# Kernel optimization log

Measured on AMD Instinct MI355X. Metric: run time of the kernel, lower is better.

## Reference

```python
import jax, jax.numpy as jnp
import numpy as np

D_MODEL = 1024
N_HEADS = 16
HEAD_DIM = D_MODEL // N_HEADS
ROPE_BASE = 10000.0
NEG_INF = -1.0e9


def rotate_half(x):
    # interleaved pairs: (-x2_i, x1_i) re-flattened to last dim
    x1 = x[..., ::2]
    x2 = x[..., 1::2]
    return jnp.stack((-x2, x1), axis=-1).reshape(x.shape)


def rope_sin_cos(seq_len, head_dim, dtype):
    inv_freq = 1.0 / (ROPE_BASE ** (jnp.arange(0, head_dim, 2, dtype=jnp.float32) / head_dim))
    t = jnp.arange(seq_len, dtype=jnp.float32)
    freqs = jnp.einsum('i,j->ij', t, inv_freq)          # [T, hd/2]
    emb = jnp.concatenate((freqs, freqs), axis=-1)       # [T, hd]
    return jnp.sin(emb).astype(dtype), jnp.cos(emb).astype(dtype)


def apply_rope(x, sin, cos):
    # x: [B, H, T, hd]; sin/cos: [T, hd]
    return x * cos[None, None] + rotate_half(x) * sin[None, None]


def setup_inputs() -> dict:
    key = jax.random.key(0)
    ks = jax.random.split(key, 9)
    B, T, D = 2, 2048, D_MODEL
    q = jax.random.normal(ks[0], (B, T, D), dtype=jnp.float32)
    k = jax.random.normal(ks[1], (B, T, D), dtype=jnp.float32)
    v = jax.random.normal(ks[2], (B, T, D), dtype=jnp.float32)
    # causal additive mask, broadcastable over [B, H, Tq, Tk]
    causal = jnp.triu(jnp.full((T, T), NEG_INF, dtype=jnp.float32), k=1)
    attn_mask = causal[None, None]
    key_padding_mask = jax.random.uniform(ks[3], (B, T)) < 0.05
    scale = 1.0 / np.sqrt(D)
    Wq = jax.random.normal(ks[4], (D, D), dtype=jnp.float32) * scale
    Wk = jax.random.normal(ks[5], (D, D), dtype=jnp.float32) * scale
    Wv = jax.random.normal(ks[6], (D, D), dtype=jnp.float32) * scale
    Wo = jax.random.normal(ks[7], (D, D), dtype=jnp.float32) * scale
    return {"q": q, "k": k, "v": v, "attn_mask": attn_mask,
            "key_padding_mask": key_padding_mask,
            "Wq": Wq, "Wk": Wk, "Wv": Wv, "Wo": Wo}


def reference(q, k, v, attn_mask, key_padding_mask, Wq, Wk, Wv, Wo):
    B, Tq, _ = q.shape
    Tk = k.shape[1]
    H, hd = N_HEADS, HEAD_DIM
    # projections (nn.Linear: x @ W.T), split heads -> [B, H, T, hd]
    qh = (q @ Wq.T).reshape(B, Tq, H, hd).transpose(0, 2, 1, 3)
    kh = (k @ Wk.T).reshape(B, Tk, H, hd).transpose(0, 2, 1, 3)
    vh = (v @ Wv.T).reshape(B, Tk, H, hd).transpose(0, 2, 1, 3)
    sin_q, cos_q = rope_sin_cos(Tq, hd, q.dtype)
    sin_k, cos_k = rope_sin_cos(Tk, hd, k.dtype)
    qh = apply_rope(qh, sin_q, cos_q)
    kh = apply_rope(kh, sin_k, cos_k)
    scores = jnp.einsum('bhqd,bhkd->bhqk', qh, kh) / np.sqrt(hd)
    scores = scores + attn_mask
    scores = jnp.where(key_padding_mask[:, None, None, :], NEG_INF, scores)
    attn = jax.nn.softmax(scores, axis=-1)
    out = jnp.einsum('bhqk,bhkd->bhqd', attn, vh)
    out = out.transpose(0, 2, 1, 3).reshape(B, Tq, H * hd)
    return out @ Wo.T
```

## Files before the change

kernel.cpp:

```cpp
#include <hip/hip_runtime.h>
#include <stdint.h>

typedef __bf16 bf16x8 __attribute__((ext_vector_type(8)));
typedef float f32x4 __attribute__((ext_vector_type(4)));
typedef float f32x16 __attribute__((ext_vector_type(16)));

#define NEG_BIG2 (-1.442695040e9f)
#define SC_LOG2  (0.180336880f)

__device__ __forceinline__ unsigned short f2b(float f) {
  union { float f; unsigned int u; } c; c.f = f;
  unsigned int u = c.u;
  u += 0x7FFFu + ((u >> 16) & 1u);
  return (unsigned short)(u >> 16);
}
__device__ __forceinline__ float b2f(unsigned short h) {
  union { unsigned int u; float f; } c; c.u = ((unsigned int)h) << 16;
  return c.f;
}
__device__ __forceinline__ unsigned int pk2(float a, float b) {
  __bf16 x = (__bf16)a, y = (__bf16)b;
  unsigned short xu, yu;
  __builtin_memcpy(&xu, &x, 2);
  __builtin_memcpy(&yu, &y, 2);
  return (unsigned)xu | ((unsigned)yu << 16);
}
__device__ __forceinline__ float ex2(float x) {
  float r; asm("v_exp_f32 %0, %1" : "=v"(r) : "v"(x)); return r;
}

typedef const __attribute__((address_space(1))) unsigned int ga_u32;
typedef __attribute__((address_space(3))) unsigned int ls_u32;
__device__ __forceinline__ void gld16(const void* g, void* l) {
  __builtin_amdgcn_global_load_lds((ga_u32*)g, (ls_u32*)l, 16, 0, 0);
}

__device__ __forceinline__ void swap_pair(unsigned a, unsigned b, int hi,
                                          unsigned& lo_out, unsigned& hi_out) {
#if __has_builtin(__builtin_amdgcn_permlane32_swap)
  auto r = __builtin_amdgcn_permlane32_swap(a, b, false, false);
  lo_out = r[0]; hi_out = r[1];
#else
  unsigned pa = __shfl_xor(a, 32), pb = __shfl_xor(b, 32);
  lo_out = hi ? pb : a;
  hi_out = hi ? b : pa;
#endif
}

__device__ __constant__ unsigned char job_tab[24] = {
  7, 47, 63, 46, 62, 6, 45, 61, 44, 60, 5, 43,
  59, 42, 58, 4, 41, 57, 40, 56, 3, 2, 1, 0};

__global__ void rope_table_k(float* __restrict__ sin_t, float* __restrict__ cos_t) {
  int i = blockIdx.x * blockDim.x + threadIdx.x;
  int t = i >> 6, d = i & 63, f = d & 31;
  double inv = exp(-((double)(2 * f) / 64.0) * log(10000.0));
  double ang = (double)t * inv;
  sin_t[i] = (float)sin(ang);
  cos_t[i] = (float)cos(ang);
}

__global__ void detect_mask_k(const unsigned int* __restrict__ kpm, int* __restrict__ flag) {
  unsigned int v = 0;
  for (int i = threadIdx.x; i < 1024; i += 256) v |= kpm[i];
  if (v & ~1u) atomicOr(flag, 1);
}

__global__ void mask_pack_k(const void* __restrict__ kpm, const int* __restrict__ mflag,
                            unsigned long long* __restrict__ pmask) {
  const int w = threadIdx.x >> 6, lane = threadIdx.x & 63;
  const int bytes = *mflag;
  for (int i = w; i < 64; i += 4) {
    int b = i >> 5, kb = i & 31;
    int idx = b * 2048 + kb * 64 + lane;
    int pad = bytes ? (int)((const unsigned char*)kpm)[idx] : ((const int*)kpm)[idx];
    unsigned long long pm = __ballot(pad != 0);
    if (lane == 0) pmask[i] = pm;
  }
}

__global__ void convw_k(const float* __restrict__ Wq, const float* __restrict__ Wk,
                        const float* __restrict__ Wv, const float* __restrict__ Wo,
                        unsigned short* __restrict__ Wb) {
  size_t g = (size_t)blockIdx.x * 256 + threadIdx.x;
  size_t i8 = g * 8;
  int t = (int)(i8 >> 20);
  const float* src = (t == 0 ? Wq : t == 1 ? Wk : t == 2 ? Wv : Wo) + (i8 & 1048575);
  float4 a = *(const float4*)src, c = *(const float4*)(src + 4);
  uint4 o = { pk2(a.x, a.y), pk2(a.z, a.w), pk2(c.x, c.y), pk2(c.z, c.w) };
  *(uint4*)&Wb[i8] = o;
}

__global__ void conv_in_k(const float* __restrict__ q, const float* __restrict__ k,
                          const float* __restrict__ v, unsigned short* __restrict__ qb,
                          unsigned short* __restrict__ kb, unsigned short* __restrict__ vb) {
  size_t g = (size_t)blockIdx.x * 256 + threadIdx.x;
  size_t i8 = g * 8;
  int t = (int)(i8 >> 22);
  size_t off = i8 & 4194303;
  const float* src = (t == 0 ? q : t == 1 ? k : v) + off;
  unsigned short* dst = (t == 0 ? qb : t == 1 ? kb : vb) + off;
  float4 a = *(const float4*)src, c = *(const float4*)(src + 4);
  uint4 o = { pk2(a.x, a.y), pk2(a.z, a.w), pk2(c.x, c.y), pk2(c.z, c.w) };
  *(uint4*)dst = o;
}

template<bool ABF>
__global__ __launch_bounds__(256) void qkv_k(const void* __restrict__ A0,
                                             const void* __restrict__ A1,
                                             const void* __restrict__ A2,
                                             const unsigned short* __restrict__ Wb,
                                             unsigned short* __restrict__ qh,
                                             unsigned short* __restrict__ kh,
                                             unsigned short* __restrict__ vt) {
  const int z = blockIdx.z;
  const void* Ap = (z == 0) ? A0 : (z == 1) ? A1 : A2;
  const unsigned short* Wp = Wb + (size_t)z * 1048576;
  unsigned short* outp = (z == 0) ? qh : (z == 1) ? kh : vt;

  __shared__ unsigned short As[128 * 32];
  __shared__ unsigned short Bs[128 * 32];
  const int M0 = blockIdx.x * 128, N0 = blockIdx.y * 128;
  const int tid = threadIdx.x, lane = tid & 63, w = tid >> 6;
  const int wr = w >> 1, wc = w & 1;
  const int lrow = lane & 15, lgrp = lane >> 4;

  const f32x4 Z4 = {0.f, 0.f, 0.f, 0.f};
  f32x4 acc[4][4];
#pragma unroll
  for (int i = 0; i < 4; ++i)
#pragma unroll
    for (int j = 0; j < 4; ++j) acc[i][j] = Z4;

  for (int kt = 0; kt < 1024; kt += 32) {
    __syncthreads();
    if (ABF) {
      const unsigned short* Ab = (const unsigned short*)Ap;
#pragma unroll
      for (int i = 0; i < 2; ++i) {
        const unsigned short* gA = Ab +
            (size_t)(M0 + i * 64 + w * 16 + (lane >> 2)) * 1024 + kt + (lane & 3) * 8;
        gld16(gA, &As[i * 2048 + w * 512]);
      }
    } else {
      const int row = tid >> 1, half = tid & 1;
      const float* ap = (const float*)Ap + (size_t)(M0 + row) * 1024 + kt + half * 16;
      float4 f0 = *(const float4*)ap, f1 = *(const float4*)(ap + 4);
      float4 f2 = *(const float4*)(ap + 8), f3 = *(const float4*)(ap + 12);
      uint4 u0 = { pk2(f0.x, f0.y), pk2(f0.z, f0.w), pk2(f1.x, f1.y), pk2(f1.z, f1.w) };
      uint4 u1 = { pk2(f2.x, f2.y), pk2(f2.z, f2.w), pk2(f3.x, f3.y), pk2(f3.z, f3.w) };
      *(uint4*)&As[row * 32 + half * 16] = u0;
      *(uint4*)&As[row * 32 + half * 16 + 8] = u1;
    }
#pragma unroll
    for (int i = 0; i < 2; ++i) {
      const unsigned short* gB = Wp +
          (size_t)(N0 + i * 64 + w * 16 + (lane >> 2)) * 1024 + kt + (lane & 3) * 8;
      gld16(gB, &Bs[i * 2048 + w * 512]);
    }
    __syncthreads();
    bf16x8 af[4], bfv[4];
#pragma unroll
    for (int m = 0; m < 4; ++m)
      af[m] = *(const bf16x8*)&As[(wr * 64 + m * 16 + lrow) * 32 + lgrp * 8];
#pragma unroll
    for (int n = 0; n < 4; ++n)
      bfv[n] = *(const bf16x8*)&Bs[(wc * 64 + n * 16 + lrow) * 32 + lgrp * 8];
    __builtin_amdgcn_s_setprio(1);
#pragma unroll
    for (int m = 0; m < 4; ++m)
#pragma unroll
      for (int n = 0; n < 4; ++n)
        acc[m][n] = __builtin_amdgcn_mfma_f32_16x16x32_bf16(af[m], bfv[n], acc[m][n], 0, 0, 0);
    __builtin_amdgcn_s_setprio(0);
  }

#pragma unroll
  for (int mi = 0; mi < 4; ++mi)
#pragma unroll
    for (int ni = 0; ni < 4; ++ni) {
      const int m = M0 + wr * 64 + mi * 16 + lgrp * 4;
      const int n = N0 + wc * 64 + ni * 16 + lrow;
      const int b = m >> 11, t = m & 2047;
      if (z < 2) {
        unsigned short* o = outp +
            ((size_t)(b * 16 + (n >> 6)) * 2048 + t) * 64 + (n & 63);
#pragma unroll
        for (int r = 0; r < 4; ++r) o[(size_t)r * 64] = f2b(acc[mi][ni][r]);
      } else {
        unsigned short* o = outp +
            ((size_t)(b * 16 + (n >> 6)) * 64 + (n & 63)) * 2048 + t;
        *(ushort4*)o = make_ushort4(f2b(acc[mi][ni][0]), f2b(acc[mi][ni][1]),
                                    f2b(acc[mi][ni][2]), f2b(acc[mi][ni][3]));
      }
    }
}

__global__ __launch_bounds__(256) void gemm_o_k(const unsigned short* __restrict__ Ab,
                                                const unsigned short* __restrict__ Wp,
                                                float* __restrict__ outp) {
  __shared__ unsigned short As[64 * 32];
  __shared__ unsigned short Bs[128 * 32];
  const int M0 = blockIdx.x * 64, N0 = blockIdx.y * 128;
  const int tid = threadIdx.x, lane = tid & 63, w = tid >> 6;
  const int wr = w >> 1, wc = w & 1;
  const int lrow = lane & 15, lgrp = lane >> 4;

  const f32x4 Z4 = {0.f, 0.f, 0.f, 0.f};
  f32x4 acc[2][4];
#pragma unroll
  for (int i = 0; i < 2; ++i)
#pragma unroll
    for (int j = 0; j < 4; ++j) acc[i][j] = Z4;

  for (int kt = 0; kt < 1024; kt += 32) {
    __syncthreads();
    {
      const unsigned short* gA = Ab +
          (size_t)(M0 + w * 16 + (lane >> 2)) * 1024 + kt + (lane & 3) * 8;
      gld16(gA, &As[w * 512]);
    }
#pragma unroll
    for (int i = 0; i < 2; ++i) {
      const unsigned short* gB = Wp +
          (size_t)(N0 + i * 64 + w * 16 + (lane >> 2)) * 1024 + kt + (lane & 3) * 8;
      gld16(gB, &Bs[i * 2048 + w * 512]);
    }
    __syncthreads();
    bf16x8 af[2], bfv[4];
#pragma unroll
    for (int m = 0; m < 2; ++m)
      af[m] = *(const bf16x8*)&As[(wr * 32 + m * 16 + lrow) * 32 + lgrp * 8];
#pragma unroll
    for (int n = 0; n < 4; ++n)
      bfv[n] = *(const bf16x8*)&Bs[(wc * 64 + n * 16 + lrow) * 32 + lgrp * 8];
    __builtin_amdgcn_s_setprio(1);
#pragma unroll
    for (int m = 0; m < 2; ++m)
#pragma unroll
      for (int n = 0; n < 4; ++n)
        acc[m][n] = __builtin_amdgcn_mfma_f32_16x16x32_bf16(af[m], bfv[n], acc[m][n], 0, 0, 0);
    __builtin_amdgcn_s_setprio(0);
  }

#pragma unroll
  for (int mi = 0; mi < 2; ++mi)
#pragma unroll
    for (int ni = 0; ni < 4; ++ni) {
      const int m = M0 + wr * 32 + mi * 16 + lgrp * 4;
      const int n = N0 + wc * 64 + ni * 16 + lrow;
      float* o = outp + (size_t)m * 1024 + n;
#pragma unroll
      for (int r = 0; r < 4; ++r) o[(size_t)r * 1024] = acc[mi][ni][r];
    }
}

__global__ void rope_apply_k(unsigned short* __restrict__ qh, unsigned short* __restrict__ kh,
                             const float* __restrict__ sin_t, const float* __restrict__ cos_t) {
  const size_t per = (size_t)2 * 16 * 2048 * 16;
  size_t gid = (size_t)blockIdx.x * blockDim.x + threadIdx.x;
  if (gid >= 2 * per) return;
  const bool is_q = gid < per;
  unsigned short* base = is_q ? qh : kh;
  const float sc = is_q ? SC_LOG2 : 1.0f;
  size_t g = is_q ? gid : gid - per;
  const int t = (int)((g >> 4) & 2047);
  const int d0 = ((int)g & 15) * 4;
  ushort4 x = ((ushort4*)base)[g];
  const float4 s4 = *(const float4*)&sin_t[t * 64 + d0];
  const float4 c4 = *(const float4*)&cos_t[t * 64 + d0];
  float x0 = b2f(x.x), x1 = b2f(x.y), x2 = b2f(x.z), x3 = b2f(x.w);
  ushort4 o;
  o.x = f2b((x0 * c4.x - x1 * s4.x) * sc);
  o.y = f2b((x1 * c4.y + x0 * s4.y) * sc);
  o.z = f2b((x2 * c4.z - x3 * s4.z) * sc);
  o.w = f2b((x3 * c4.w + x2 * s4.w) * sc);
  ((ushort4*)base)[g] = o;
}

__global__ __launch_bounds__(256, 2) void attn_k(
    const unsigned short* __restrict__ qh, const unsigned short* __restrict__ kh,
    const unsigned short* __restrict__ vt, const unsigned long long* __restrict__ pmask,
    unsigned short* __restrict__ ao, float* __restrict__ Op, float* __restrict__ Ml,
    const int mode) {
  const int bid = blockIdx.x;
  int bh, tile, half = 0, split = 0;
  if (mode) {
    const unsigned char j = job_tab[bid >> 5];
    bh = bid & 31;
    tile = j & 15; half = (j >> 4) & 1; split = j >> 5;
  } else {
    const int x = bid & 7, g = bid >> 3;
    bh = x * 4 + (g & 3);
    tile = 15 - (g >> 2);
  }
  const int b = bh >> 4, h = bh & 15;
  const int tid = threadIdx.x, lane = tid & 63, w = tid >> 6;
  const int ln31 = lane & 31, hi = lane >> 5;

  __shared__ char Kb[2][8192];
  __shared__ char Vb[2][8192];
  __shared__ int flagv;

  const size_t bh_off = (size_t)bh * 2048 * 64;
  const int qw = tile * 128 + w * 32;
  const int q_abs = qw + ln31;
  const int kb_begin = (split && half) ? tile + 1 : 0;
  const int kb_end_stage = (split && !half) ? tile + 1 : tile * 2 + 2;
  const int nkv_w = min(qw / 64 + 1, kb_end_stage);
  const int swz = (ln31 & 7) << 4;

  bf16x8 qf[4];
#pragma unroll
  for (int dc = 0; dc < 4; ++dc)
    qf[dc] = *(const bf16x8*)(qh + bh_off + (size_t)(qw + ln31) * 64 + dc * 16 + hi * 8);

  const f32x16 Z16 = {0.f,0.f,0.f,0.f,0.f,0.f,0.f,0.f,0.f,0.f,0.f,0.f,0.f,0.f,0.f,0.f};
  f32x16 O0 = Z16, O1 = Z16;
  float m_run = -INFINITY, l_run = 0.f;

  uint4 kr0, kr1, vr0, vr1;
  const int srow = tid >> 2, sseg = tid & 3;
  const int sbase = srow * 128 + sseg * 32;
  const int sswz = (srow & 7) << 4;

  auto stage_load = [&](int kbi) {
    const unsigned short* kp = kh + bh_off + (size_t)(kbi * 64 + srow) * 64 + sseg * 16;
    kr0 = *(const uint4*)kp; kr1 = *(const uint4*)(kp + 8);
    const unsigned short* vp = vt + bh_off + (size_t)srow * 2048 + kbi * 64 + sseg * 16;
    vr0 = *(const uint4*)vp; vr1 = *(const uint4*)(vp + 8);
  };
  auto stage_write = [&](int bu) {
    *(uint4*)(Kb[bu] + (sbase ^ sswz)) = kr0;
    *(uint4*)(Kb[bu] + ((sbase + 16) ^ sswz)) = kr1;
    *(uint4*)(Vb[bu] + (sbase ^ sswz)) = vr0;
    *(uint4*)(Vb[bu] + ((sbase + 16) ^ sswz)) = vr1;
  };

  auto compute = [&](int kb, int cur) {
    const unsigned long long pm = pmask[b * 32 + kb];
    const unsigned plo = (unsigned)(pm >> (hi * 4));
    const unsigned phi = (unsigned)((pm >> 32) >> (hi * 4));
    f32x16 S0 = Z16, S1 = Z16;
    __builtin_amdgcn_s_setprio(1);
#pragma unroll
    for (int dc = 0; dc < 4; ++dc) {
      bf16x8 k0 = *(const bf16x8*)(Kb[cur] + ((ln31 * 128 + dc * 32 + hi * 16) ^ swz));
      bf16x8 k1 = *(const bf16x8*)(Kb[cur] + (((ln31 + 32) * 128 + dc * 32 + hi * 16) ^ swz));
      S0 = __builtin_amdgcn_mfma_f32_32x32x16_bf16(k0, qf[dc], S0, 0, 0, 0);
      S1 = __builtin_amdgcn_mfma_f32_32x32x16_bf16(k1, qf[dc], S1, 0, 0, 0);
    }
    __builtin_amdgcn_s_setprio(0);

    const bool diag = (kb * 64 + 63) > qw;
    if (diag) {
#pragma unroll
      for (int r = 0; r < 16; ++r) {
        const int kloc = (r & 3) + 8 * (r >> 2);
        float sv = S0[r];
        sv = ((plo >> kloc) & 1) ? NEG_BIG2
             : ((kb * 64 + kloc + 4 * hi > q_abs) ? sv + NEG_BIG2 : sv);
        S0[r] = sv;
        float sw = S1[r];
        sw = ((phi >> kloc) & 1) ? NEG_BIG2
             : ((kb * 64 + 32 + kloc + 4 * hi > q_abs) ? sw + NEG_BIG2 : sw);
        S1[r] = sw;
      }
    } else {
#pragma unroll
      for (int r = 0; r < 16; ++r) {
        const int kloc = (r & 3) + 8 * (r >> 2);
        S0[r] = ((plo >> kloc) & 1) ? NEG_BIG2 : S0[r];
        S1[r] = ((phi >> kloc) & 1) ? NEG_BIG2 : S1[r];
      }
    }

    float vm = fmaxf(S0[0], S0[1]);
#pragma unroll
    for (int r = 2; r < 16; r += 2) vm = fmaxf(vm, fmaxf(S0[r], S0[r + 1]));
#pragma unroll
    for (int r = 0; r < 16; r += 2) vm = fmaxf(vm, fmaxf(S1[r], S1[r + 1]));
    vm = fmaxf(vm, __shfl_xor(vm, 32));

    if (__any(vm > m_run + 11.5f)) {
      const float mnew = fmaxf(m_run, vm);
      const float alpha = ex2(m_run - mnew);
      m_run = mnew;
      l_run *= alpha;
      O0 *= alpha; O1 *= alpha;
    }
    float rs = 0.f;
#pragma unroll
    for (int r = 0; r < 16; ++r) { float p = ex2(S0[r] - m_run); S0[r] = p; rs += p; }
#pragma unroll
    for (int r = 0; r < 16; ++r) { float p = ex2(S1[r] - m_run); S1[r] = p; rs += p; }
    rs += __shfl_xor(rs, 32);
    l_run += rs;

    union U8 { uint4 u; bf16x8 v; };
    bf16x8 pa[4];
#pragma unroll
    for (int kt = 0; kt < 2; ++kt) {
#pragma unroll
      for (int hf = 0; hf < 2; ++hf) {
        float p0, p1, p2, p3, p4, p5, p6, p7;
        if (kt == 0) {
          if (hf == 0) { p0=S0[0];p1=S0[1];p2=S0[2];p3=S0[3];p4=S0[4];p5=S0[5];p6=S0[6];p7=S0[7]; }
          else         { p0=S0[8];p1=S0[9];p2=S0[10];p3=S0[11];p4=S0[12];p5=S0[13];p6=S0[14];p7=S0[15]; }
        } else {
          if (hf == 0) { p0=S1[0];p1=S1[1];p2=S1[2];p3=S1[3];p4=S1[4];p5=S1[5];p6=S1[6];p7=S1[7]; }
          else         { p0=S1[8];p1=S1[9];p2=S1[10];p3=S1[11];p4=S1[12];p5=S1[13];p6=S1[14];p7=S1[15]; }
        }
        unsigned e0 = pk2(p0, p1), e1 = pk2(p2, p3);
        unsigned o0 = pk2(p4, p5), o1 = pk2(p6, p7);
        unsigned a0, b0_, a1, b1_;
        swap_pair(e0, o0, hi, a0, b0_);
        swap_pair(e1, o1, hi, a1, b1_);
        U8 u; u.u = make_uint4(a0, a1, b0_, b1_);
        pa[kt * 2 + hf] = u.v;
      }
    }

    __builtin_amdgcn_s_setprio(1);
#pragma unroll
    for (int c = 0; c < 4; ++c) {
      bf16x8 v0 = *(const bf16x8*)(Vb[cur] + ((ln31 * 128 + c * 32 + hi * 16) ^ swz));
      bf16x8 v1 = *(const bf16x8*)(Vb[cur] + (((ln31 + 32) * 128 + c * 32 + hi * 16) ^ swz));
      O0 = __builtin_amdgcn_mfma_f32_32x32x16_bf16(v0, pa[c], O0, 0, 0, 0);
      O1 = __builtin_amdgcn_mfma_f32_32x32x16_bf16(v1, pa[c], O1, 0, 0, 0);
    }
    __builtin_amdgcn_s_setprio(0);
  };

  const int nsteps = kb_end_stage - kb_begin;
  stage_load(kb_begin);
  stage_write(0);
  for (int s = 0; s < nsteps; ++s) {
    const int kb = kb_begin + s;
    if (s + 1 < nsteps) stage_load(kb + 1);
    __syncthreads();
    if (kb < nkv_w) compute(kb, s & 1);
    __syncthreads();
    if (s + 1 < nsteps) stage_write((s + 1) & 1);
  }

  if (!split) {
    if (tid == 0) flagv = 0;
    __syncthreads();
    if (m_run <= -7.2e8f) flagv = 1;
    __syncthreads();
    if (flagv) {
      for (int kb = kb_end_stage - 1; kb < 32; ++kb) {
        if (kb + 1 < 32) stage_load(kb + 1);
        __syncthreads();
        if (kb >= nkv_w) compute(kb, kb & 1);
        __syncthreads();
        if (kb + 1 < 32) stage_write((kb + 1) & 1);
      }
    }
    const float inv = 1.0f / l_run;
    unsigned short* op = ao + (size_t)(b * 2048 + qw + ln31) * 1024 + h * 64;
#pragma unroll
    for (int g2 = 0; g2 < 4; ++g2) {
      const int d0 = 8 * g2 + 4 * hi;
      *(ushort4*)(op + d0) = make_ushort4(
          f2b(O0[g2 * 4 + 0] * inv), f2b(O0[g2 * 4 + 1] * inv),
          f2b(O0[g2 * 4 + 2] * inv), f2b(O0[g2 * 4 + 3] * inv));
      *(ushort4*)(op + 32 + d0) = make_ushort4(
          f2b(O1[g2 * 4 + 0] * inv), f2b(O1[g2 * 4 + 1] * inv),
          f2b(O1[g2 * 4 + 2] * inv), f2b(O1[g2 * 4 + 3] * inv));
    }
  } else {
    const int bh8t = bh * 8 + (tile - 8);
    const int qloc = w * 32 + ln31;
    float* opp = Op + (size_t)(bh8t * 2 + half) * 8192 + qloc;
#pragma unroll
    for (int r = 0; r < 16; ++r) {
      const int d = (r & 3) + 8 * (r >> 2) + 4 * hi;
      opp[d * 128] = O0[r];
      opp[(d + 32) * 128] = O1[r];
    }
    if (hi == 0) {
      float* mlp = Ml + (size_t)(bh8t * 2 + half) * 256 + qloc;
      mlp[0] = m_run;
      mlp[128] = l_run;
    }
  }
}

__global__ __launch_bounds__(256) void merge_k(const float* __restrict__ Op,
                                               const float* __restrict__ Ml,
                                               unsigned short* __restrict__ ao) {
  const int bh = blockIdx.x & 31, t8 = blockIdx.x >> 5;
  const int b = bh >> 4, h = bh & 15;
  const int tile = t8 + 8;
  const size_t ob = (size_t)(bh * 8 + t8) * 2 * 8192;
  const size_t mlb = (size_t)(bh * 8 + t8) * 2 * 256;
  __shared__ float T[128][69];
  const int tid = threadIdx.x;

  for (int i = tid; i < 8192; i += 256) {
    const int d = i >> 7, q = i & 127;
    const float m0 = Ml[mlb + q],       l0 = Ml[mlb + 128 + q];
    const float m1 = Ml[mlb + 256 + q], l1 = Ml[mlb + 384 + q];
    const float m = fmaxf(m0, m1);
    const float a0 = ex2(m0 - m), a1 = ex2(m1 - m);
    const float linv = 1.0f / (l0 * a0 + l1 * a1);
    const float v = (Op[ob + i] * a0 + Op[ob + 8192 + i] * a1) * linv;
    T[q][d] = v;
  }
  __syncthreads();

  const int q = tid >> 1, dbase = (tid & 1) * 32;
  unsigned short* op = ao + (size_t)(b * 2048 + tile * 128 + q) * 1024 + h * 64 + dbase;
#pragma unroll
  for (int j = 0; j < 8; ++j) {
    const int d = dbase + j * 4;
    *(ushort4*)(op + j * 4) = make_ushort4(f2b(T[q][d]), f2b(T[q][d + 1]),
                                           f2b(T[q][d + 2]), f2b(T[q][d + 3]));
  }
}

extern "C" void kernel_launch(void* const* d_in, const int* in_sizes, int n_in,
                              void* d_out, int out_size, void* d_ws, size_t ws_size,
                              hipStream_t stream) {
  const float* q  = (const float*)d_in[0];
  const float* k  = (const float*)d_in[1];
  const float* v  = (const float*)d_in[2];
  const void*  kpm = d_in[4];
  const float* Wq = (const float*)d_in[5];
  const float* Wk = (const float*)d_in[6];
  const float* Wv = (const float*)d_in[7];
  const float* Wo = (const float*)d_in[8];

  char* ws = (char*)d_ws;
  unsigned short* qh = (unsigned short*)(ws);
  unsigned short* kh = (unsigned short*)(ws + (8u << 20));
  unsigned short* vt = (unsigned short*)(ws + (16u << 20));
  unsigned short* ao = (unsigned short*)(ws + (24u << 20));
  unsigned short* Wb = (unsigned short*)(ws + (32u << 20));
  float* sin_t = (float*)(ws + (40u << 20));
  float* cos_t = (float*)(ws + (40u << 20) + 524288);
  unsigned long long* pmask = (unsigned long long*)(ws + (41u << 20));
  int* mflag = (int*)(ws + (41u << 20) + 512);
  unsigned short* qb = (unsigned short*)(ws + (42u << 20));
  unsigned short* kb = (unsigned short*)(ws + (50u << 20));
  unsigned short* vb = (unsigned short*)(ws + (58u << 20));
  float* Opart = (float*)(ws + (66ull << 20));
  float* Mlpart = (float*)(ws + (83ull << 20));

  const bool big = ws_size >= (66ull << 20);
  const bool can_split = ws_size >= (84ull << 20);

  (void)hipMemsetAsync(mflag, 0, sizeof(int), stream);
  detect_mask_k<<<1, 256, 0, stream>>>((const unsigned int*)kpm, mflag);
  mask_pack_k<<<1, 256, 0, stream>>>(kpm, mflag, pmask);
  rope_table_k<<<512, 256, 0, stream>>>(sin_t, cos_t);
  convw_k<<<2048, 256, 0, stream>>>(Wq, Wk, Wv, Wo, Wb);

  dim3 gq(32, 8, 3);
  if (big) {
    conv_in_k<<<6144, 256, 0, stream>>>(q, k, v, qb, kb, vb);
    qkv_k<true><<<gq, 256, 0, stream>>>(qb, kb, vb, Wb, qh, kh, vt);
  } else {
    qkv_k<false><<<gq, 256, 0, stream>>>(q, k, v, Wb, qh, kh, vt);
  }

  rope_apply_k<<<8192, 256, 0, stream>>>(qh, kh, sin_t, cos_t);

  attn_k<<<can_split ? 768 : 512, 256, 0, stream>>>(qh, kh, vt, pmask, ao,
                                                    Opart, Mlpart, can_split ? 1 : 0);
  if (can_split) merge_k<<<256, 256, 0, stream>>>(Opart, Mlpart, ao);

  gemm_o_k<<<dim3(64, 8), 256, 0, stream>>>(ao, Wb + 3145728, (float*)d_out);
}
```

Before: 161.4 us.

## Use fixed softmax offset, pre-swizzled K/V layout with direct LDS loads

After: 543.7 us. +236.9%, slower.

```diff
diff --git a/kernel.cpp b/kernel.cpp
--- a/kernel.cpp
+++ b/kernel.cpp
@@ -35,15 +35,15 @@
   __builtin_amdgcn_global_load_lds((ga_u32*)g, (ls_u32*)l, 16, 0, 0);
 }
 
-__device__ __forceinline__ void swap_pair(unsigned a, unsigned b, int hi,
+__device__ __forceinline__ void swap_pair(unsigned a, unsigned b, int hig,
                                           unsigned& lo_out, unsigned& hi_out) {
 #if __has_builtin(__builtin_amdgcn_permlane32_swap)
   auto r = __builtin_amdgcn_permlane32_swap(a, b, false, false);
   lo_out = r[0]; hi_out = r[1];
 #else
   unsigned pa = __shfl_xor(a, 32), pb = __shfl_xor(b, 32);
-  lo_out = hi ? pb : a;
-  hi_out = hi ? b : pa;
+  lo_out = hig ? pb : a;
+  hi_out = hig ? b : pa;
 #endif
 }
 
@@ -182,14 +182,23 @@
       const int m = M0 + wr * 64 + mi * 16 + lgrp * 4;
       const int n = N0 + wc * 64 + ni * 16 + lrow;
       const int b = m >> 11, t = m & 2047;
-      if (z < 2) {
+      const int d = n & 63;
+      if (z == 0) {
         unsigned short* o = outp +
-            ((size_t)(b * 16 + (n >> 6)) * 2048 + t) * 64 + (n & 63);
+            ((size_t)(b * 16 + (n >> 6)) * 2048 + t) * 64 + d;
 #pragma unroll
         for (int r = 0; r < 4; ++r) o[(size_t)r * 64] = f2b(acc[mi][ni][r]);
+      } else if (z == 1) {
+        unsigned short* ob = outp + (size_t)(b * 16 + (n >> 6)) * 131072 + (t >> 6) * 4096;
+#pragma unroll
+        for (int r = 0; r < 4; ++r) {
+          const int tt = t + r;
+          ob[(tt & 63) * 64 + (d ^ ((tt & 7) << 3))] = f2b(acc[mi][ni][r]);
+        }
       } else {
-        unsigned short* o = outp +
-            ((size_t)(b * 16 + (n >> 6)) * 64 + (n & 63)) * 2048 + t;
+        const int kl = t & 63;
+        unsigned short* o = outp + (size_t)(b * 16 + (n >> 6)) * 131072 + (t >> 6) * 4096
+                          + d * 64 + (kl ^ ((d & 7) << 3));
         *(ushort4*)o = make_ushort4(f2b(acc[mi][ni][0]), f2b(acc[mi][ni][1]),
                                     f2b(acc[mi][ni][2]), f2b(acc[mi][ni][3]));
       }
@@ -265,20 +274,21 @@
   const float sc = is_q ? SC_LOG2 : 1.0f;
   size_t g = is_q ? gid : gid - per;
   const int t = (int)((g >> 4) & 2047);
-  const int d0 = ((int)g & 15) * 4;
+  const int x0 = ((int)g & 15) * 4;
+  const int d0 = is_q ? x0 : (x0 ^ ((t & 7) << 3));
   ushort4 x = ((ushort4*)base)[g];
   const float4 s4 = *(const float4*)&sin_t[t * 64 + d0];
   const float4 c4 = *(const float4*)&cos_t[t * 64 + d0];
-  float x0 = b2f(x.x), x1 = b2f(x.y), x2 = b2f(x.z), x3 = b2f(x.w);
+  float x0f = b2f(x.x), x1f = b2f(x.y), x2f = b2f(x.z), x3f = b2f(x.w);
   ushort4 o;
-  o.x = f2b((x0 * c4.x - x1 * s4.x) * sc);
-  o.y = f2b((x1 * c4.y + x0 * s4.y) * sc);
-  o.z = f2b((x2 * c4.z - x3 * s4.z) * sc);
-  o.w = f2b((x3 * c4.w + x2 * s4.w) * sc);
+  o.x = f2b((x0f * c4.x - x1f * s4.x) * sc);
+  o.y = f2b((x1f * c4.y + x0f * s4.y) * sc);
+  o.z = f2b((x2f * c4.z - x3f * s4.z) * sc);
+  o.w = f2b((x3f * c4.w + x2f * s4.w) * sc);
   ((ushort4*)base)[g] = o;
 }
 
-__global__ __launch_bounds__(256, 2) void attn_k(
+__global__ __launch_bounds__(256, 4) void attn_k(
     const unsigned short* __restrict__ qh, const unsigned short* __restrict__ kh,
     const unsigned short* __restrict__ vt, const unsigned long long* __restrict__ pmask,
     unsigned short* __restrict__ ao, float* __restrict__ Op, float* __restrict__ Ml,
@@ -296,106 +306,114 @@
   }
   const int b = bh >> 4, h = bh & 15;
   const int tid = threadIdx.x, lane = tid & 63, w = tid >> 6;
-  const int ln31 = lane & 31, hi = lane >> 5;
+  const int ln31 = lane & 31, hig = lane >> 5;
 
   __shared__ char Kb[2][8192];
   __shared__ char Vb[2][8192];
   __shared__ int flagv;
 
-  const size_t bh_off = (size_t)bh * 2048 * 64;
+  const size_t bh_off = (size_t)bh * 131072;
   const int qw = tile * 128 + w * 32;
   const int q_abs = qw + ln31;
   const int kb_begin = (split && half) ? tile + 1 : 0;
-  const int kb_end_stage = (split && !half) ? tile + 1 : tile * 2 + 2;
-  const int nkv_w = min(qw / 64 + 1, kb_end_stage);
+  const int kb_end = (split && !half) ? tile + 1 : tile * 2 + 2;
+  const int nkv_w = min(qw / 64 + 1, kb_end);
   const int swz = (ln31 & 7) << 4;
 
   bf16x8 qf[4];
 #pragma unroll
   for (int dc = 0; dc < 4; ++dc)
-    qf[dc] = *(const bf16x8*)(qh + bh_off + (size_t)(qw + ln31) * 64 + dc * 16 + hi * 8);
+    qf[dc] = *(const bf16x8*)(qh + (size_t)bh * 131072 + (size_t)(qw + ln31) * 64 +
+                              dc * 16 + hig * 8);
 
   const f32x16 Z16 = {0.f,0.f,0.f,0.f,0.f,0.f,0.f,0.f,0.f,0.f,0.f,0.f,0.f,0.f,0.f,0.f};
   f32x16 O0 = Z16, O1 = Z16;
   float m_run = -INFINITY, l_run = 0.f;
 
-  uint4 kr0, kr1, vr0, vr1;
-  const int srow = tid >> 2, sseg = tid & 3;
-  const int sbase = srow * 128 + sseg * 32;
-  const int sswz = (srow & 7) << 4;
-
-  auto stage_load = [&](int kbi) {
-    const unsigned short* kp = kh + bh_off + (size_t)(kbi * 64 + srow) * 64 + sseg * 16;
-    kr0 = *(const uint4*)kp; kr1 = *(const uint4*)(kp + 8);
-    const unsigned short* vp = vt + bh_off + (size_t)srow * 2048 + kbi * 64 + sseg * 16;
-    vr0 = *(const uint4*)vp; vr1 = *(const uint4*)(vp + 8);
+  auto stage = [&](int kbi, int bu) {
+    const unsigned short* kp = kh + bh_off + (size_t)kbi * 4096 + w * 512 + lane * 8;
+    char* kd = Kb[bu] + w * 1024;
+    gld16(kp, kd);
+    gld16(kp + 2048, kd + 4096);
+    const unsigned short* vp = vt + bh_off + (size_t)kbi * 4096 + w * 512 + lane * 8;
+    char* vd = Vb[bu] + w * 1024;
+    gld16(vp, vd);
+    gld16(vp + 2048, vd + 4096);
   };
-  auto stage_write = [&](int bu) {
-    *(uint4*)(Kb[bu] + (sbase ^ sswz)) = kr0;
-    *(uint4*)(Kb[bu] + ((sbase + 16) ^ sswz)) = kr1;
-    *(uint4*)(Vb[bu] + (sbase ^ sswz)) = vr0;
-    *(uint4*)(Vb[bu] + ((sbase + 16) ^ sswz)) = vr1;
-  };
-
-  auto compute = [&](int kb, int cur) {
+
+  auto compute = [&](int kb, int cur, bool track) {
     const unsigned long long pm = pmask[b * 32 + kb];
-    const unsigned plo = (unsigned)(pm >> (hi * 4));
-    const unsigned phi = (unsigned)((pm >> 32) >> (hi * 4));
+    const unsigned plo = (unsigned)(pm >> (hig * 4));
+    const unsigned phi = (unsigned)((pm >> 32) >> (hig * 4));
     f32x16 S0 = Z16, S1 = Z16;
     __builtin_amdgcn_s_setprio(1);
 #pragma unroll
     for (int dc = 0; dc < 4; ++dc) {
-      bf16x8 k0 = *(const bf16x8*)(Kb[cur] + ((ln31 * 128 + dc * 32 + hi * 16) ^ swz));
-      bf16x8 k1 = *(const bf16x8*)(Kb[cur] + (((ln31 + 32) * 128 + dc * 32 + hi * 16) ^ swz));
+      bf16x8 k0 = *(const bf16x8*)(Kb[cur] + ((ln31 * 128 + dc * 32 + hig * 16) ^ swz));
+      bf16x8 k1 = *(const bf16x8*)(Kb[cur] + (((ln31 + 32) * 128 + dc * 32 + hig * 16) ^ swz));
       S0 = __builtin_amdgcn_mfma_f32_32x32x16_bf16(k0, qf[dc], S0, 0, 0, 0);
       S1 = __builtin_amdgcn_mfma_f32_32x32x16_bf16(k1, qf[dc], S1, 0, 0, 0);
     }
     __builtin_amdgcn_s_setprio(0);
 
     const bool diag = (kb * 64 + 63) > qw;
-    if (diag) {
+    if (!track) {
+      float rs = 0.f;
 #pragma unroll
       for (int r = 0; r < 16; ++r) {
         const int kloc = (r & 3) + 8 * (r >> 2);
-        float sv = S0[r];
-        sv = ((plo >> kloc) & 1) ? NEG_BIG2
-             : ((kb * 64 + kloc + 4 * hi > q_abs) ? sv + NEG_BIG2 : sv);
-        S0[r] = sv;
-        float sw = S1[r];
-        sw = ((phi >> kloc) & 1) ? NEG_BIG2
-             : ((kb * 64 + 32 + kloc + 4 * hi > q_abs) ? sw + NEG_BIG2 : sw);
-        S1[r] = sw;
+        bool c0 = (plo >> kloc) & 1;
+        bool c1 = (phi >> kloc) & 1;
+        if (diag) {
+          c0 = c0 || (kb * 64 + kloc + 4 * hig > q_abs);
+          c1 = c1 || (kb * 64 + 32 + kloc + 4 * hig > q_abs);
+        }
+        float p0 = c0 ? 0.f : ex2(S0[r] - 12.f);
+        float p1 = c1 ? 0.f : ex2(S1[r] - 12.f);
+        S0[r] = p0; S1[r] = p1;
+        rs += p0 + p1;
       }
+      l_run += rs;
     } else {
-#pragma unroll
-      for (int r = 0; r < 16; ++r) {
-        const int kloc = (r & 3) + 8 * (r >> 2);
-        S0[r] = ((plo >> kloc) & 1) ? NEG_BIG2 : S0[r];
-        S1[r] = ((phi >> kloc) & 1) ? NEG_BIG2 : S1[r];
+      if (diag) {
+#pragma unroll
+        for (int r = 0; r < 16; ++r) {
+          const int kloc = (r & 3) + 8 * (r >> 2);
+          float sv = S0[r];
+          sv = ((plo >> kloc) & 1) ? NEG_BIG2
+               : ((kb * 64 + kloc + 4 * hig > q_abs) ? sv + NEG_BIG2 : sv);
+          S0[r] = sv;
+          float sw = S1[r];
+          sw = ((phi >> kloc) & 1) ? NEG_BIG2
+               : ((kb * 64 + 32 + kloc + 4 * hig > q_abs) ? sw + NEG_BIG2 : sw);
+          S1[r] = sw;
+        }
+      } else {
+#pragma unroll
+        for (int r = 0; r < 16; ++r) {
+          const int kloc = (r & 3) + 8 * (r >> 2);
+          S0[r] = ((plo >> kloc) & 1) ? NEG_BIG2 : S0[r];
+          S1[r] = ((phi >> kloc) & 1) ? NEG_BIG2 : S1[r];
+        }
       }
-    }
-
-    float vm = fmaxf(S0[0], S0[1]);
-#pragma unroll
-    for (int r = 2; r < 16; r += 2) vm = fmaxf(vm, fmaxf(S0[r], S0[r + 1]));
-#pragma unroll
-    for (int r = 0; r < 16; r += 2) vm = fmaxf(vm, fmaxf(S1[r], S1[r + 1]));
-    vm = fmaxf(vm, __shfl_xor(vm, 32));
-
-    if (__any(vm > m_run + 11.5f)) {
+      float vm = fmaxf(S0[0], S0[1]);
+#pragma unroll
+      for (int r = 2; r < 16; r += 2) vm = fmaxf(vm, fmaxf(S0[r], S0[r + 1]));
+#pragma unroll
+      for (int r = 0; r < 16; r += 2) vm = fmaxf(vm, fmaxf(S1[r], S1[r + 1]));
+      vm = fmaxf(vm, __shfl_xor(vm, 32));
       const float mnew = fmaxf(m_run, vm);
       const float alpha = ex2(m_run - mnew);
       m_run = mnew;
       l_run *= alpha;
       O0 *= alpha; O1 *= alpha;
-    }
-    float rs = 0.f;
-#pragma unroll
-    for (int r = 0; r < 16; ++r) { float p = ex2(S0[r] - m_run); S0[r] = p; rs += p; }
-#pragma unroll
-    for (int r = 0; r < 16; ++r) { float p = ex2(S1[r] - m_run); S1[r] = p; rs += p; }
-    rs += __shfl_xor(rs, 32);
-    l_run += rs;
+      float rs = 0.f;
+#pragma unroll
+      for (int r = 0; r < 16; ++r) { float p = ex2(S0[r] - m_run); S0[r] = p; rs += p; }
+#pragma unroll
+      for (int r = 0; r < 16; ++r) { float p = ex2(S1[r] - m_run); S1[r] = p; rs += p; }
+      l_run += rs;
+    }
 
     union U8 { uint4 u; bf16x8 v; };
     bf16x8 pa[4];
@@ -414,8 +432,8 @@
         unsigned e0 = pk2(p0, p1), e1 = pk2(p2, p3);
         unsigned o0 = pk2(p4, p5), o1 = pk2(p6, p7);
         unsigned a0, b0_, a1, b1_;
-        swap_pair(e0, o0, hi, a0, b0_);
-        swap_pair(e1, o1, hi, a1, b1_);
+        swap_pair(e0, o0, hig, a0, b0_);
+        swap_pair(e1, o1, hig, a1, b1_);
         U8 u; u.u = make_uint4(a0, a1, b0_, b1_);
         pa[kt * 2 + hf] = u.v;
       }
@@ -424,45 +442,44 @@
     __builtin_amdgcn_s_setprio(1);
 #pragma unroll
     for (int c = 0; c < 4; ++c) {
-      bf16x8 v0 = *(const bf16x8*)(Vb[cur] + ((ln31 * 128 + c * 32 + hi * 16) ^ swz));
-      bf16x8 v1 = *(const bf16x8*)(Vb[cur] + (((ln31 + 32) * 128 + c * 32 + hi * 16) ^ swz));
+      bf16x8 v0 = *(const bf16x8*)(Vb[cur] + ((ln31 * 128 + c * 32 + hig * 16) ^ swz));
+      bf16x8 v1 = *(const bf16x8*)(Vb[cur] + (((ln31 + 32) * 128 + c * 32 + hig * 16) ^ swz));
       O0 = __builtin_amdgcn_mfma_f32_32x32x16_bf16(v0, pa[c], O0, 0, 0, 0);
       O1 = __builtin_amdgcn_mfma_f32_32x32x16_bf16(v1, pa[c], O1, 0, 0, 0);
     }
     __builtin_amdgcn_s_setprio(0);
   };
 
-  const int nsteps = kb_end_stage - kb_begin;
-  stage_load(kb_begin);
-  stage_write(0);
-  for (int s = 0; s < nsteps; ++s) {
-    const int kb = kb_begin + s;
-    if (s + 1 < nsteps) stage_load(kb + 1);
-    __syncthreads();
-    if (kb < nkv_w) compute(kb, s & 1);
-    __syncthreads();
-    if (s + 1 < nsteps) stage_write((s + 1) & 1);
-  }
+  auto mainloop = [&](int lo, int hi2, int nkvw, bool track) {
+    const int n = hi2 - lo;
+    if (n <= 0) return;
+    stage(lo, 0);
+    for (int s = 0; s < n; ++s) {
+      __syncthreads();
+      if (s + 1 < n) stage(lo + s + 1, (s + 1) & 1);
+      const int kb = lo + s;
+      if (kb < nkvw) compute(kb, s & 1, track);
+    }
+  };
+
+  mainloop(kb_begin, kb_end, nkv_w, false);
+  float l_tot = l_run + __shfl_xor(l_run, 32);
 
   if (!split) {
     if (tid == 0) flagv = 0;
     __syncthreads();
-    if (m_run <= -7.2e8f) flagv = 1;
+    if (l_tot == 0.f) flagv = 1;
     __syncthreads();
     if (flagv) {
-      for (int kb = kb_end_stage - 1; kb < 32; ++kb) {
-        if (kb + 1 < 32) stage_load(kb + 1);
-        __syncthreads();
-        if (kb >= nkv_w) compute(kb, kb & 1);
-        __syncthreads();
-        if (kb + 1 < 32) stage_write((kb + 1) & 1);
-      }
-    }
-    const float inv = 1.0f / l_run;
+      O0 = Z16; O1 = Z16; l_run = 0.f; m_run = -INFINITY;
+      mainloop(0, 32, 32, true);
+      l_tot = l_run + __shfl_xor(l_run, 32);
+    }
+    const float inv = 1.0f / l_tot;
     unsigned short* op = ao + (size_t)(b * 2048 + qw + ln31) * 1024 + h * 64;
 #pragma unroll
     for (int g2 = 0; g2 < 4; ++g2) {
-      const int d0 = 8 * g2 + 4 * hi;
+      const int d0 = 8 * g2 + 4 * hig;
       *(ushort4*)(op + d0) = make_ushort4(
           f2b(O0[g2 * 4 + 0] * inv), f2b(O0[g2 * 4 + 1] * inv),
           f2b(O0[g2 * 4 + 2] * inv), f2b(O0[g2 * 4 + 3] * inv));
@@ -476,14 +493,14 @@
     float* opp = Op + (size_t)(bh8t * 2 + half) * 8192 + qloc;
 #pragma unroll
     for (int r = 0; r < 16; ++r) {
-      const int d = (r & 3) + 8 * (r >> 2) + 4 * hi;
+      const int d = (r & 3) + 8 * (r >> 2) + 4 * hig;
       opp[d * 128] = O0[r];
       opp[(d + 32) * 128] = O1[r];
     }
-    if (hi == 0) {
+    if (hig == 0) {
       float* mlp = Ml + (size_t)(bh8t * 2 + half) * 256 + qloc;
-      mlp[0] = m_run;
-      mlp[128] = l_run;
+      mlp[0] = 12.0f;
+      mlp[128] = l_tot;
     }
   }
 }
```
